# Kernel tuning notes

Hardware: AMD Instinct MI355X
Metric: run time of the kernel (lower is better)

The kernel has to match this reference:

```python
import jax, jax.numpy as jnp
import numpy as np
from jax import lax

CIN, COUT, K, PAD = 256, 128, 3, 1


def setup_inputs() -> dict:
    key = jax.random.key(0)
    ks = jax.random.split(key, 5)
    N, h0, w0 = 2, 64, 64
    x = jax.random.normal(ks[0], (N, CIN, h0, w0), jnp.float32)
    lateral_feat = jax.random.normal(ks[1], (N, COUT, 1, 1), jnp.float32)
    trans_w = jax.random.normal(ks[2], (CIN, COUT, K, K), jnp.float32) * 0.02
    off_w1 = jax.random.normal(ks[3], (64, COUT, 3, 3), jnp.float32) * 0.02
    off_b1 = jnp.zeros((64,), jnp.float32)
    off_w2 = jax.random.normal(ks[4], (2 * K * K, 64, 3, 3), jnp.float32) * 0.02
    off_b2 = jnp.zeros((2 * K * K,), jnp.float32)
    return dict(x=x, lateral_feat=lateral_feat, trans_w=trans_w,
                off_w1=off_w1, off_b1=off_b1, off_w2=off_w2, off_b2=off_b2)


def _conv2d(x, w, b, pad):
    y = lax.conv_general_dilated(x, w, (1, 1), [(pad, pad), (pad, pad)],
                                 dimension_numbers=('NCHW', 'OIHW', 'NCHW'))
    return y + b[None, :, None, None]


def _conv_transpose2d(x, w, stride, pad, out_pad):
    # torch ConvTranspose2d weight layout: [Cin, Cout, k, k]
    k = w.shape[2]
    wt = jnp.flip(w, (2, 3)).transpose(1, 0, 2, 3)  # [Cout, Cin, k, k]
    lo = k - 1 - pad
    hi = k - 1 - pad + out_pad
    return lax.conv_general_dilated(x, wt, (1, 1), [(lo, hi), (lo, hi)],
                                    lhs_dilation=(stride, stride),
                                    dimension_numbers=('NCHW', 'OIHW', 'NCHW'))


def _deform_conv2d(x, offset, w, pad):
    # x [N,C,H,W], offset [N,2*K*K,H,W] (y,x interleaved per kernel tap), w [O,C,K,K]
    N, C, H, W = x.shape
    O = w.shape[0]
    KK = K * K
    off = offset.reshape(N, KK, 2, H, W)
    ky = jnp.arange(KK) // K
    kx = jnp.arange(KK) % K
    py = jnp.arange(H)[None, None, :, None] + (ky - pad)[None, :, None, None] + off[:, :, 0]
    px = jnp.arange(W)[None, None, None, :] + (kx - pad)[None, :, None, None] + off[:, :, 1]
    y0 = jnp.floor(py)
    x0 = jnp.floor(px)
    dy = py - y0
    dx = px - x0
    y0i = y0.astype(jnp.int32)
    x0i = x0.astype(jnp.int32)
    xf = x.reshape(N, C, H * W)

    def corner(yi, xi, wgt):
        valid = (yi >= 0) & (yi < H) & (xi >= 0) & (xi < W)
        idx = (jnp.clip(yi, 0, H - 1) * W + jnp.clip(xi, 0, W - 1)).reshape(N, -1)
        v = jnp.take_along_axis(xf, idx[:, None, :], axis=2).reshape(N, C, KK, H, W)
        return v * (wgt * valid)[:, None]

    sampled = (corner(y0i, x0i, (1 - dy) * (1 - dx))
               + corner(y0i, x0i + 1, (1 - dy) * dx)
               + corner(y0i + 1, x0i, dy * (1 - dx))
               + corner(y0i + 1, x0i + 1, dy * dx))  # [N,C,KK,H,W]
    return jnp.einsum('nckhw,ock->nohw', sampled, w.reshape(O, C, KK))


def reference(x, lateral_feat, trans_w, off_w1, off_b1, off_w2, off_b2):
    up = _conv_transpose2d(x, trans_w, 2, PAD, 1)          # [N, COUT, 2h0, 2w0]
    h = jax.nn.relu(_conv2d(lateral_feat, off_w1, off_b1, 1))
    offset = jnp.tanh(_conv2d(h, off_w2, off_b2, 1))       # [N, 18, 1, 1]
    N, C, H, W = up.shape
    # offset.repeat(1, 1, H, W) with 1x1 spatial input == broadcast to full grid
    offset = jnp.broadcast_to(offset, (N, 2 * K * K, H, W))
    # deform_conv2d uses trans_conv weight [O=CIN, I=COUT, K, K], stride=1, pad=PAD
    return _deform_conv2d(up, offset, trans_w, PAD)        # [N, CIN, H, W]
```

## Files before the change

### kernel.cpp

```cpp
#include <hip/hip_runtime.h>
#include <hip/hip_bf16.h>
#include <math.h>

typedef __attribute__((ext_vector_type(8))) short s16x8;
typedef __attribute__((ext_vector_type(4))) float f32x4;

__device__ __forceinline__ unsigned short f2bf(float f) {
    union { float f; unsigned int u; } v; v.f = f;
    unsigned int u = v.u + 0x7FFFu + ((v.u >> 16) & 1u);
    return (unsigned short)(u >> 16);
}
__device__ __forceinline__ unsigned pk2(float lo, float hi) {
    __hip_bfloat162 h = __float22bfloat162_rn(make_float2(lo, hi));
    union { __hip_bfloat162 h; unsigned u; } v; v.h = h;
    return v.u;
}
__device__ __forceinline__ float blo(unsigned u) {
    union { unsigned u; float f; } v; v.u = u << 16; return v.f;
}
__device__ __forceinline__ float bhi(unsigned u) {
    union { unsigned u; float f; } v; v.u = u & 0xffff0000u; return v.f;
}

__device__ __forceinline__ void blend_store(uint4 uA, uint4 uB, uint4 uC, uint4 uD,
                                            float4 cw, unsigned short* dst) {
    unsigned ua[4] = {uA.x, uA.y, uA.z, uA.w};
    unsigned ub[4] = {uB.x, uB.y, uB.z, uB.w};
    unsigned uc[4] = {uC.x, uC.y, uC.z, uC.w};
    unsigned ud[4] = {uD.x, uD.y, uD.z, uD.w};
    unsigned pk[4];
#pragma unroll
    for (int i = 0; i < 4; ++i) {
        float vL = cw.x * blo(ua[i]) + cw.y * blo(ub[i]) + cw.z * blo(uc[i]) + cw.w * blo(ud[i]);
        float vH = cw.x * bhi(ua[i]) + cw.y * bhi(ub[i]) + cw.z * bhi(uc[i]) + cw.w * bhi(ud[i]);
        pk[i] = pk2(vL, vH);
    }
    *(uint4*)dst = make_uint4(pk[0], pk[1], pk[2], pk[3]);
}

__global__ __launch_bounds__(256) void k_prep(const float* __restrict__ x,
                                              const float* __restrict__ lat,
                                              const float* __restrict__ tw,
                                              const float* __restrict__ w1,
                                              const float* __restrict__ b1,
                                              const float* __restrict__ w2,
                                              const float* __restrict__ b2,
                                              unsigned short* __restrict__ xp,
                                              unsigned short* __restrict__ A2f,
                                              unsigned short* __restrict__ Awf,
                                              int* __restrict__ ipar,
                                              float* __restrict__ fpar) {
    __shared__ float sm[8420];
    int b = blockIdx.x, t = threadIdx.x;
    if (b == 0) {
        for (int i = t; i < 8192; i += 256) sm[(i >> 7) * 129 + (i & 127)] = w1[i * 9 + 4];
        __syncthreads();
        if (t < 128) {
            int n = t >> 6, o = t & 63;
            float s = b1[o];
            const float* ln = lat + n * 128;
#pragma unroll 8
            for (int c = 0; c < 128; ++c) s += ln[c] * sm[o * 129 + c];
            sm[8256 + t] = fmaxf(s, 0.f);
        }
        __syncthreads();
        if (t < 36) {
            int n = t / 18, j = t % 18;
            float s = b2[j];
            for (int o = 0; o < 64; ++o) s += sm[8256 + n * 64 + o] * w2[(j * 64 + o) * 9 + 4];
            float ov = tanhf(s);
            ov = fminf(fmaxf(ov, -0.999999f), 0.999999f);
            sm[8384 + t] = ov;
        }
        __syncthreads();
        if (t < 36) {
            int n = t / 18, j = t % 18;
            int tap = j >> 1, d = j & 1;
            float ov = sm[8384 + t];
            float fl = floorf(ov);
            int kc = d ? (tap % 3) : (tap / 3);
            ipar[(n * 9 + tap) * 2 + d] = kc - 1 + (int)fl;
            fpar[(n * 9 + tap) * 2 + d] = ov - fl;
        }
    } else if (b < 145) {
        int slot = (b - 1) * 256 + t;
        int l = slot & 63;
        int mi = (slot >> 6) & 3;
        int w = (slot >> 8) & 3;
        int k = slot >> 10;
        int row = w * 64 + mi * 16 + (l & 15);
        int kq = l >> 4;
        unsigned short v[8];
#pragma unroll
        for (int j = 0; j < 8; ++j) {
            int kcol = k * 32 + kq * 8 + j;
            int tap = kcol >> 7, c = kcol & 127;
            v[j] = f2bf(tw[(row * 128 + c) * 9 + tap]);
        }
        unsigned p0 = (unsigned)v[0] | ((unsigned)v[1] << 16);
        unsigned p1 = (unsigned)v[2] | ((unsigned)v[3] << 16);
        unsigned p2 = (unsigned)v[4] | ((unsigned)v[5] << 16);
        unsigned p3 = (unsigned)v[6] | ((unsigned)v[7] << 16);
        *(uint4*)(A2f + slot * 8) = make_uint4(p0, p1, p2, p3);
    } else if (b < 289) {
        int slot = (b - 145) * 256 + t;
        int l = slot & 63;
        int mi = (slot >> 6) & 3;
        int wm = (slot >> 8) & 1;
        int k = slot >> 9;
        int row = wm * 64 + mi * 16 + (l & 15);
        int kq = l >> 4;
        unsigned short v[8];
#pragma unroll
        for (int j = 0; j < 8; ++j) {
            int kcol = k * 32 + kq * 8 + j;
            int t9 = kcol >> 8, ci = kcol & 255;
            int ky = t9 / 3, kx = t9 - ky * 3;
            v[j] = f2bf(tw[(ci * 128 + row) * 9 + (2 - ky) * 3 + (2 - kx)]);
        }
        unsigned p0 = (unsigned)v[0] | ((unsigned)v[1] << 16);
        unsigned p1 = (unsigned)v[2] | ((unsigned)v[3] << 16);
        unsigned p2 = (unsigned)v[4] | ((unsigned)v[5] << 16);
        unsigned p3 = (unsigned)v[6] | ((unsigned)v[7] << 16);
        *(uint4*)(Awf + slot * 8) = make_uint4(p0, p1, p2, p3);
    } else {
        int bb = b - 289;
        int h = bb & 63, cq = (bb >> 6) & 3, n = bb >> 8;
        int c0 = cq * 64;
        {
            int wcol = t & 63, sub = t >> 6;
            for (int r = 0; r < 16; ++r) {
                int ci_l = r * 4 + sub;
                sm[ci_l * 65 + wcol] = x[((n * 256 + c0 + ci_l) * 64 + h) * 64 + wcol];
            }
        }
        __syncthreads();
        int wcol = t >> 2, cg = t & 3;
        unsigned short* dst = xp + (size_t)n * (65 * 65 * 256) + (h * 65 + wcol) * 256 + c0 + cg * 16;
        unsigned pk[8];
#pragma unroll
        for (int j = 0; j < 8; ++j)
            pk[j] = pk2(sm[(cg * 16 + 2 * j) * 65 + wcol], sm[(cg * 16 + 2 * j + 1) * 65 + wcol]);
        *(uint4*)dst = make_uint4(pk[0], pk[1], pk[2], pk[3]);
        *(uint4*)(dst + 8) = make_uint4(pk[4], pk[5], pk[6], pk[7]);
    }
}

__global__ __launch_bounds__(256) void k_tconv3(const unsigned short* __restrict__ xp,
                                                const unsigned short* __restrict__ Awf,
                                                unsigned short* __restrict__ upp) {
    __shared__ unsigned short Bs[2][64][40];
    __shared__ int st9[4];
    __shared__ int sbb[4];
    int t = threadIdx.x;
    int b = blockIdx.x;
    int phase = b >> 8, jj = b & 255;
    int n = jj >> 7, xpar = ((jj >> 6) & 1) ^ phase, yh = jj & 63;
    int y = yh * 2 + phase;
    const unsigned short* xpn = xp + (size_t)n * (65 * 65 * 256);

    int lane = t & 63, w = t >> 6;
    int col = lane & 15, q = lane >> 4;
    int wm = w >> 1, wn = w & 1;
    int bx = t >> 2, bcg = t & 3;
    int boff = bx * 256 + bcg * 8;

    int kys[2], kxs[2], nky, nkx;
    if (phase) { kys[0] = 0; kys[1] = 2; nky = 2; } else { kys[0] = 1; kys[1] = 1; nky = 1; }
    if (xpar)  { kxs[0] = 0; kxs[1] = 2; nkx = 2; } else { kxs[0] = 1; kxs[1] = 1; nkx = 1; }
    int nslots = nky * nkx;
    if (t < nslots) {
        int a1 = t / nkx, a2 = t % nkx;
        int ky = kys[a1], kx = kxs[a2];
        st9[t] = ky * 3 + kx;
        int d2 = (y + ky - 1) >> 1;
        int s = (xpar + kx - 1) >> 1;
        sbb[t] = (d2 * 65 + s) * 256;
    }
    int NT = nslots * 8;

    f32x4 acc[4][2];
#pragma unroll
    for (int mi = 0; mi < 4; ++mi)
#pragma unroll
        for (int ni = 0; ni < 2; ++ni) acc[mi][ni] = (f32x4){0.f, 0.f, 0.f, 0.f};

    __syncthreads();

    const unsigned short* Afw = Awf + wm * 2048 + lane * 8;
    s16x8 a_cur[4], a_nxt[4];

    {
        int kAw0 = st9[0] * 8;
        uint4 bv = *(const uint4*)(xpn + sbb[0] + boff);
        *(uint4*)&Bs[0][bx][bcg * 8] = bv;
#pragma unroll
        for (int mi = 0; mi < 4; ++mi)
            a_cur[mi] = *(const s16x8*)(Afw + kAw0 * 4096 + mi * 512);
    }
    __syncthreads();

    for (int cc = 0; cc < NT; ++cc) {
        int cc1 = cc + 1;
        uint4 bv;
        if (cc1 < NT) {
            int slot1 = cc1 >> 3, cb1 = cc1 & 7;
            int t9v = st9[slot1];
            int base = sbb[slot1];
            bv = *(const uint4*)(xpn + base + cb1 * 32 + boff);
            int kAw1 = t9v * 8 + cb1;
#pragma unroll
            for (int mi = 0; mi < 4; ++mi)
                a_nxt[mi] = *(const s16x8*)(Afw + kAw1 * 4096 + mi * 512);
        }
        s16x8 bb[2];
#pragma unroll
        for (int ni = 0; ni < 2; ++ni)
            bb[ni] = *(const s16x8*)&Bs[cc & 1][wn * 32 + ni * 16 + col][q * 8];
#pragma unroll
        for (int mi = 0; mi < 4; ++mi)
#pragma unroll
            for (int ni = 0; ni < 2; ++ni)
                acc[mi][ni] = __builtin_amdgcn_mfma_f32_16x16x32_bf16(a_cur[mi], bb[ni], acc[mi][ni], 0, 0, 0);
        if (cc1 < NT) {
            *(uint4*)&Bs[cc1 & 1][bx][bcg * 8] = bv;
#pragma unroll
            for (int mi = 0; mi < 4; ++mi) a_cur[mi] = a_nxt[mi];
        }
        __syncthreads();
    }

    unsigned short* uppn = upp + (size_t)n * (132 * 132 * 128);
#pragma unroll
    for (int mi = 0; mi < 4; ++mi)
#pragma unroll
        for (int ni = 0; ni < 2; ++ni) {
            int co = wm * 64 + mi * 16 + q * 4;
            int p64 = wn * 32 + ni * 16 + col;
            int xg = 2 * p64 + xpar;
            unsigned short* p = uppn + ((y + 2) * 132 + (xg + 2)) * 128 + co;
            unsigned lo = pk2(acc[mi][ni][0], acc[mi][ni][1]);
            unsigned hi = pk2(acc[mi][ni][2], acc[mi][ni][3]);
            *(uint2*)p = make_uint2(lo, hi);
        }
}

__global__ __launch_bounds__(256) void k_deform3(const unsigned short* __restrict__ upp,
                                                 const unsigned short* __restrict__ A2f,
                                                 const int* __restrict__ ipar,
                                                 const float* __restrict__ fpar,
                                                 float* __restrict__ out) {
    __shared__ unsigned short Bs[2][64][40];
    __shared__ int sbase[9];
    __shared__ float4 swt[9];
    int t = threadIdx.x;
    int b = blockIdx.x;
    int xcd = b & 7, j = b >> 3;
    int n = xcd >> 2, band = xcd & 3;
    int y = band * 32 + (j & 31);
    int tx0 = (j >> 5) * 64;
    const unsigned short* uppn = upp + (size_t)n * (132 * 132 * 128);

    int lane = t & 63, w = t >> 6;
    int col = lane & 15, q = lane >> 4;
    int bx = t >> 2, bcg = t & 3;
    int boff = bx * 128 + bcg * 8;

    if (t < 9) {
        int iy = ipar[(n * 9 + t) * 2 + 0], ix = ipar[(n * 9 + t) * 2 + 1];
        float fy = fpar[(n * 9 + t) * 2 + 0], fx = fpar[(n * 9 + t) * 2 + 1];
        sbase[t] = ((y + 2 + iy) * 132 + (tx0 + 2 + ix)) * 128;
        swt[t] = make_float4((1.f - fy) * (1.f - fx), (1.f - fy) * fx, fy * (1.f - fx), fy * fx);
    }

    f32x4 acc[4][4];
#pragma unroll
    for (int mi = 0; mi < 4; ++mi)
#pragma unroll
        for (int ni = 0; ni < 4; ++ni) acc[mi][ni] = (f32x4){0.f, 0.f, 0.f, 0.f};

    __syncthreads();

    const unsigned short* Afw = A2f + w * 2048 + lane * 8;
    s16x8 a_cur[4], a_nxt[4];

    {
        const unsigned short* p = uppn + sbase[0] + boff;
        uint4 uA = *(const uint4*)p;
        uint4 uB = *(const uint4*)(p + 128);
        uint4 uC = *(const uint4*)(p + 16896);
        uint4 uD = *(const uint4*)(p + 17024);
        blend_store(uA, uB, uC, uD, swt[0], &Bs[0][bx][bcg * 8]);
#pragma unroll
        for (int mi = 0; mi < 4; ++mi)
            a_cur[mi] = *(const s16x8*)(Afw + mi * 512);
    }
    __syncthreads();

#pragma unroll 2
    for (int k = 0; k < 36; ++k) {
        int k1 = k + 1;
        uint4 uA, uB, uC, uD;
        float4 cw;
        if (k1 < 36) {
            int t1 = k1 >> 2, cb1 = (k1 & 3) * 32;
            int base = sbase[t1];
            cw = swt[t1];
            const unsigned short* p = uppn + base + cb1 + boff;
            uA = *(const uint4*)p;
            uB = *(const uint4*)(p + 128);
            uC = *(const uint4*)(p + 16896);
            uD = *(const uint4*)(p + 17024);
#pragma unroll
            for (int mi = 0; mi < 4; ++mi)
                a_nxt[mi] = *(const s16x8*)(Afw + k1 * 8192 + mi * 512);
        }
        s16x8 bb[4];
#pragma unroll
        for (int ni = 0; ni < 4; ++ni)
            bb[ni] = *(const s16x8*)&Bs[k & 1][ni * 16 + col][q * 8];
#pragma unroll
        for (int mi = 0; mi < 4; ++mi)
#pragma unroll
            for (int ni = 0; ni < 4; ++ni)
                acc[mi][ni] = __builtin_amdgcn_mfma_f32_16x16x32_bf16(a_cur[mi], bb[ni], acc[mi][ni], 0, 0, 0);
        if (k1 < 36) {
            blend_store(uA, uB, uC, uD, cw, &Bs[k1 & 1][bx][bcg * 8]);
#pragma unroll
            for (int mi = 0; mi < 4; ++mi) a_cur[mi] = a_nxt[mi];
        }
        __syncthreads();
    }

#pragma unroll
    for (int mi = 0; mi < 4; ++mi)
#pragma unroll
        for (int ni = 0; ni < 4; ++ni) {
            int o = w * 64 + mi * 16 + q * 4;
            int xg = tx0 + ni * 16 + col;
            float* p = out + (((size_t)(n * 256 + o)) * 128 + y) * 128 + xg;
            p[0]         = acc[mi][ni][0];
            p[16384]     = acc[mi][ni][1];
            p[2 * 16384] = acc[mi][ni][2];
            p[3 * 16384] = acc[mi][ni][3];
        }
}

extern "C" void kernel_launch(void* const* d_in, const int* in_sizes, int n_in,
                              void* d_out, int out_size, void* d_ws, size_t ws_size,
                              hipStream_t stream) {
    const float* x   = (const float*)d_in[0];
    const float* lat = (const float*)d_in[1];
    const float* tw  = (const float*)d_in[2];
    const float* w1  = (const float*)d_in[3];
    const float* b1  = (const float*)d_in[4];
    const float* w2  = (const float*)d_in[5];
    const float* b2  = (const float*)d_in[6];
    float* out = (float*)d_out;

    char* ws = (char*)d_ws;
    unsigned short* upp = (unsigned short*)ws;
    unsigned short* xp  = (unsigned short*)(ws + 8921088);
    unsigned short* A2f = (unsigned short*)(ws + 13247488);
    unsigned short* Awf = (unsigned short*)(ws + 13837312);
    int*   ipar         = (int*)(ws + 14427136);
    float* fpar         = (float*)(ws + 14427424);

    hipMemsetAsync(ws, 0, 13247488, stream);
    k_prep<<<801, 256, 0, stream>>>(x, lat, tw, w1, b1, w2, b2, xp, A2f, Awf, ipar, fpar);
    k_tconv3<<<512, 256, 0, stream>>>(xp, Awf, upp);
    k_deform3<<<512, 256, 0, stream>>>(upp, A2f, ipar, fpar, out);
}
```

Baseline: 150.0 us.

## Deepen global prefetch to two stages and use lighter barriers in GEMM loops

Both the transposed-conv and deformable-conv MFMA loops now prefetch global B data two iterations ahead into rotating register sets. The loops are manually unrolled by two, which removes register moves between the A-fragment buffers. __syncthreads is replaced by an LDS-only waitcnt plus s_barrier, so outstanding global loads no longer stall at each barrier. The tconv block index mapping is also reordered so neighbouring blocks share phase and parity, and the bilinear blend is written with 2-wide float vectors. The cost is extra register pressure from the additional prefetch buffers, which could reduce occupancy.

```diff
diff --git a/kernel.cpp b/kernel.cpp
--- a/kernel.cpp
+++ b/kernel.cpp
@@ -4,6 +4,7 @@
 
 typedef __attribute__((ext_vector_type(8))) short s16x8;
 typedef __attribute__((ext_vector_type(4))) float f32x4;
+typedef __attribute__((ext_vector_type(2))) float f32x2;
 
 __device__ __forceinline__ unsigned short f2bf(float f) {
     union { float f; unsigned int u; } v; v.f = f;
@@ -21,6 +22,9 @@
 __device__ __forceinline__ float bhi(unsigned u) {
     union { unsigned u; float f; } v; v.u = u & 0xffff0000u; return v.f;
 }
+
+#define BARRIER() do { asm volatile("s_waitcnt lgkmcnt(0)" ::: "memory"); \
+                       __builtin_amdgcn_s_barrier(); } while (0)
 
 __device__ __forceinline__ void blend_store(uint4 uA, uint4 uB, uint4 uC, uint4 uD,
                                             float4 cw, unsigned short* dst) {
@@ -31,11 +35,25 @@
     unsigned pk[4];
 #pragma unroll
     for (int i = 0; i < 4; ++i) {
-        float vL = cw.x * blo(ua[i]) + cw.y * blo(ub[i]) + cw.z * blo(uc[i]) + cw.w * blo(ud[i]);
-        float vH = cw.x * bhi(ua[i]) + cw.y * bhi(ub[i]) + cw.z * bhi(uc[i]) + cw.w * bhi(ud[i]);
-        pk[i] = pk2(vL, vH);
+        f32x2 va = {blo(ua[i]), bhi(ua[i])};
+        f32x2 vb = {blo(ub[i]), bhi(ub[i])};
+        f32x2 vc = {blo(uc[i]), bhi(uc[i])};
+        f32x2 vd = {blo(ud[i]), bhi(ud[i])};
+        f32x2 v = cw.x * va + cw.y * vb + cw.z * vc + cw.w * vd;
+        pk[i] = pk2(v[0], v[1]);
     }
     *(uint4*)dst = make_uint4(pk[0], pk[1], pk[2], pk[3]);
+}
+
+struct C4 { uint4 A, B, C, D; };
+
+__device__ __forceinline__ C4 ldc(const unsigned short* p) {
+    C4 r;
+    r.A = *(const uint4*)p;
+    r.B = *(const uint4*)(p + 128);
+    r.C = *(const uint4*)(p + 16896);
+    r.D = *(const uint4*)(p + 17024);
+    return r;
 }
 
 __global__ __launch_bounds__(256) void k_prep(const float* __restrict__ x,
@@ -154,8 +172,10 @@
     __shared__ int sbb[4];
     int t = threadIdx.x;
     int b = blockIdx.x;
-    int phase = b >> 8, jj = b & 255;
-    int n = jj >> 7, xpar = ((jj >> 6) & 1) ^ phase, yh = jj & 63;
+    int phase = b & 1;
+    int xpar = ((b >> 1) & 1) ^ phase;
+    int n = (b >> 2) & 1;
+    int yh = b >> 3;
     int y = yh * 2 + phase;
     const unsigned short* xpn = xp + (size_t)n * (65 * 65 * 256);
 
@@ -188,47 +208,50 @@
     __syncthreads();
 
     const unsigned short* Afw = Awf + wm * 2048 + lane * 8;
-    s16x8 a_cur[4], a_nxt[4];
+    s16x8 aC[4], aN[4];
+    uint4 R0, R1;
+
+#define TCADDR(cc) (xpn + sbb[(cc) >> 3] + ((cc) & 7) * 32 + boff)
 
     {
-        int kAw0 = st9[0] * 8;
-        uint4 bv = *(const uint4*)(xpn + sbb[0] + boff);
-        *(uint4*)&Bs[0][bx][bcg * 8] = bv;
-#pragma unroll
-        for (int mi = 0; mi < 4; ++mi)
-            a_cur[mi] = *(const s16x8*)(Afw + kAw0 * 4096 + mi * 512);
-    }
-    __syncthreads();
-
-    for (int cc = 0; cc < NT; ++cc) {
-        int cc1 = cc + 1;
-        uint4 bv;
-        if (cc1 < NT) {
-            int slot1 = cc1 >> 3, cb1 = cc1 & 7;
-            int t9v = st9[slot1];
-            int base = sbb[slot1];
-            bv = *(const uint4*)(xpn + base + cb1 * 32 + boff);
-            int kAw1 = t9v * 8 + cb1;
-#pragma unroll
-            for (int mi = 0; mi < 4; ++mi)
-                a_nxt[mi] = *(const s16x8*)(Afw + kAw1 * 4096 + mi * 512);
-        }
-        s16x8 bb[2];
-#pragma unroll
-        for (int ni = 0; ni < 2; ++ni)
-            bb[ni] = *(const s16x8*)&Bs[cc & 1][wn * 32 + ni * 16 + col][q * 8];
-#pragma unroll
-        for (int mi = 0; mi < 4; ++mi)
-#pragma unroll
-            for (int ni = 0; ni < 2; ++ni)
-                acc[mi][ni] = __builtin_amdgcn_mfma_f32_16x16x32_bf16(a_cur[mi], bb[ni], acc[mi][ni], 0, 0, 0);
-        if (cc1 < NT) {
-            *(uint4*)&Bs[cc1 & 1][bx][bcg * 8] = bv;
-#pragma unroll
-            for (int mi = 0; mi < 4; ++mi) a_cur[mi] = a_nxt[mi];
-        }
-        __syncthreads();
-    }
+        R0 = *(const uint4*)TCADDR(0);
+        R1 = *(const uint4*)TCADDR(1);
+        const unsigned short* ap = Afw + st9[0] * 8 * 4096;
+#pragma unroll
+        for (int mi = 0; mi < 4; ++mi) aC[mi] = *(const s16x8*)(ap + mi * 512);
+        *(uint4*)&Bs[0][bx][bcg * 8] = R0;
+    }
+    BARRIER();
+
+#define TC_ITER(CC, BUF, AC, AN, RC, RF)                                         \
+    {                                                                            \
+        int c_ = (CC);                                                           \
+        if (c_ + 2 < NT) RF = *(const uint4*)TCADDR(c_ + 2);                     \
+        if (c_ + 1 < NT) {                                                       \
+            int s1_ = (c_ + 1) >> 3, cb1_ = (c_ + 1) & 7;                        \
+            const unsigned short* ap_ = Afw + (st9[s1_] * 8 + cb1_) * 4096;      \
+            _Pragma("unroll")                                                    \
+            for (int mi = 0; mi < 4; ++mi) AN[mi] = *(const s16x8*)(ap_ + mi * 512); \
+        }                                                                        \
+        s16x8 bb[2];                                                             \
+        _Pragma("unroll")                                                        \
+        for (int ni = 0; ni < 2; ++ni)                                           \
+            bb[ni] = *(const s16x8*)&Bs[BUF][wn * 32 + ni * 16 + col][q * 8];    \
+        _Pragma("unroll")                                                        \
+        for (int mi = 0; mi < 4; ++mi)                                           \
+            _Pragma("unroll")                                                    \
+            for (int ni = 0; ni < 2; ++ni)                                       \
+                acc[mi][ni] = __builtin_amdgcn_mfma_f32_16x16x32_bf16(AC[mi], bb[ni], acc[mi][ni], 0, 0, 0); \
+        if (c_ + 1 < NT) *(uint4*)&Bs[BUF ^ 1][bx][bcg * 8] = RC;                \
+        BARRIER();                                                               \
+    }
+
+    for (int cc = 0; cc < NT; cc += 2) {
+        TC_ITER(cc,     0, aC, aN, R1, R0);
+        TC_ITER(cc + 1, 1, aN, aC, R0, R1);
+    }
+#undef TC_ITER
+#undef TCADDR
 
     unsigned short* uppn = upp + (size_t)n * (132 * 132 * 128);
 #pragma unroll
@@ -282,55 +305,50 @@
     __syncthreads();
 
     const unsigned short* Afw = A2f + w * 2048 + lane * 8;
-    s16x8 a_cur[4], a_nxt[4];
+    s16x8 aC[4], aN[4];
+    C4 R0, R1;
+
+#define DCADDR(k) (uppn + sbase[(k) >> 2] + ((k) & 3) * 32 + boff)
 
     {
-        const unsigned short* p = uppn + sbase[0] + boff;
-        uint4 uA = *(const uint4*)p;
-        uint4 uB = *(const uint4*)(p + 128);
-        uint4 uC = *(const uint4*)(p + 16896);
-        uint4 uD = *(const uint4*)(p + 17024);
-        blend_store(uA, uB, uC, uD, swt[0], &Bs[0][bx][bcg * 8]);
-#pragma unroll
-        for (int mi = 0; mi < 4; ++mi)
-            a_cur[mi] = *(const s16x8*)(Afw + mi * 512);
-    }
-    __syncthreads();
-
-#pragma unroll 2
-    for (int k = 0; k < 36; ++k) {
-        int k1 = k + 1;
-        uint4 uA, uB, uC, uD;
-        float4 cw;
-        if (k1 < 36) {
-            int t1 = k1 >> 2, cb1 = (k1 & 3) * 32;
-            int base = sbase[t1];
-            cw = swt[t1];
-            const unsigned short* p = uppn + base + cb1 + boff;
-            uA = *(const uint4*)p;
-            uB = *(const uint4*)(p + 128);
-            uC = *(const uint4*)(p + 16896);
-            uD = *(const uint4*)(p + 17024);
-#pragma unroll
-            for (int mi = 0; mi < 4; ++mi)
-                a_nxt[mi] = *(const s16x8*)(Afw + k1 * 8192 + mi * 512);
-        }
-        s16x8 bb[4];
-#pragma unroll
-        for (int ni = 0; ni < 4; ++ni)
-            bb[ni] = *(const s16x8*)&Bs[k & 1][ni * 16 + col][q * 8];
-#pragma unroll
-        for (int mi = 0; mi < 4; ++mi)
-#pragma unroll
-            for (int ni = 0; ni < 4; ++ni)
-                acc[mi][ni] = __builtin_amdgcn_mfma_f32_16x16x32_bf16(a_cur[mi], bb[ni], acc[mi][ni], 0, 0, 0);
-        if (k1 < 36) {
-            blend_store(uA, uB, uC, uD, cw, &Bs[k1 & 1][bx][bcg * 8]);
-#pragma unroll
-            for (int mi = 0; mi < 4; ++mi) a_cur[mi] = a_nxt[mi];
-        }
-        __syncthreads();
-    }
+        R0 = ldc(DCADDR(0));
+        R1 = ldc(DCADDR(1));
+#pragma unroll
+        for (int mi = 0; mi < 4; ++mi) aC[mi] = *(const s16x8*)(Afw + mi * 512);
+        blend_store(R0.A, R0.B, R0.C, R0.D, swt[0], &Bs[0][bx][bcg * 8]);
+    }
+    BARRIER();
+
+#define DEF_ITER(KK, BUF, AC, AN, RC, RF)                                        \
+    {                                                                            \
+        int k_ = (KK);                                                           \
+        if (k_ + 2 < 36) RF = ldc(DCADDR(k_ + 2));                               \
+        if (k_ + 1 < 36) {                                                       \
+            const unsigned short* ap_ = Afw + (k_ + 1) * 8192;                   \
+            _Pragma("unroll")                                                    \
+            for (int mi = 0; mi < 4; ++mi) AN[mi] = *(const s16x8*)(ap_ + mi * 512); \
+        }                                                                        \
+        s16x8 bb[4];                                                             \
+        _Pragma("unroll")                                                        \
+        for (int ni = 0; ni < 4; ++ni)                                           \
+            bb[ni] = *(const s16x8*)&Bs[BUF][ni * 16 + col][q * 8];              \
+        _Pragma("unroll")                                                        \
+        for (int mi = 0; mi < 4; ++mi)                                           \
+            _Pragma("unroll")                                                    \
+            for (int ni = 0; ni < 4; ++ni)                                       \
+                acc[mi][ni] = __builtin_amdgcn_mfma_f32_16x16x32_bf16(AC[mi], bb[ni], acc[mi][ni], 0, 0, 0); \
+        if (k_ + 1 < 36)                                                         \
+            blend_store(RC.A, RC.B, RC.C, RC.D, swt[(k_ + 1) >> 2],              \
+                        &Bs[BUF ^ 1][bx][bcg * 8]);                              \
+        BARRIER();                                                               \
+    }
+
+    for (int kk = 0; kk < 36; kk += 2) {
+        DEF_ITER(kk,     0, aC, aN, R1, R0);
+        DEF_ITER(kk + 1, 1, aN, aC, R0, R1);
+    }
+#undef DEF_ITER
+#undef DCADDR
 
 #pragma unroll
     for (int mi = 0; mi < 4; ++mi)
```

New measurement: 146.3 us. 2.5% less time.
